# Performance work log

Measured on AMD Instinct MI355X. Metric: run time of the kernel, lower is better.

## Reference

```python
import jax, jax.numpy as jnp
import numpy as np

BLOCK_SIZE = 2048
FRAMES = 4096
BASE_RESONANCE = 0.5
MAX_GAIN = 5.0


def fft_convolve(a, b):
    # Linear convolution via zero-padded FFT, truncated to original length
    # (matches the matching-pursuit repo's fft_convolve).
    n = a.shape[-1]
    fa = jnp.fft.rfft(a, n=2 * n, axis=-1)
    fb = jnp.fft.rfft(b, n=2 * n, axis=-1)
    out = jnp.fft.irfft(fa * fb, n=2 * n, axis=-1)
    return out[..., :n]


def setup_inputs() -> dict:
    key = jax.random.key(0)
    ks = jax.random.split(key, 6)
    cp = jax.random.normal(ks[0], (1, BLOCK_SIZE, FRAMES), dtype=jnp.float32)
    w1 = jax.random.uniform(ks[1], (BLOCK_SIZE, BLOCK_SIZE), jnp.float32, -0.01, 0.01)
    w2 = jax.random.uniform(ks[2], (BLOCK_SIZE, BLOCK_SIZE), jnp.float32, -0.01, 0.01)
    audio = jax.random.uniform(ks[3], (BLOCK_SIZE, BLOCK_SIZE), jnp.float32, -0.01, 0.01)
    decays = jax.random.uniform(ks[4], (BLOCK_SIZE,), jnp.float32, 0.001, 0.99)
    gains = jax.random.uniform(ks[5], (BLOCK_SIZE,), jnp.float32, -3.0, 3.0)
    return {"cp": cp, "w1": w1, "w2": w2, "audio": audio, "decays": decays, "gains": gains}


def reference(cp, w1, w2, audio, decays, gains):
    b, c, frames = cp.shape  # b == 1, c == BLOCK_SIZE
    x0 = jnp.maximum(cp, 0.0)  # torch.relu(cp)
    # decay values in (base_resonance, 1): base + sigmoid(decays) * span
    d = BASE_RESONANCE + jax.nn.sigmoid(decays) * (1.0 - BASE_RESONANCE)  # (c,)
    g = jax.nn.sigmoid(gains) * MAX_GAIN  # (c,)

    x = jnp.einsum('ij,bjt->bit', w1, x0)  # mapping @ control_plane
    orig = x

    # decay envelope: log -> cumsum -> exp over frames => d ** (t+1)
    logd = jnp.log(1e-12 + jnp.broadcast_to(d[None, :, None], (b, c, frames)))
    denv = jnp.exp(jnp.cumsum(logd, axis=-1))  # (b, c, frames)

    x = fft_convolve(x, denv)
    x = jnp.einsum('ij,bjt->bit', w2, x) + orig
    cp_out = jnp.tanh(x * g[None, :, None])

    audio_out = jnp.einsum('wj,bjt->bwt', audio, cp_out)  # (b, window, frames)
    audio_out = jnp.transpose(audio_out, (0, 2, 1)).reshape(b, 1, -1)
    return audio_out, cp_out
```

## Files before the change

kernel.cpp:

```cpp
#include <hip/hip_runtime.h>
#include <math.h>

typedef __attribute__((ext_vector_type(8))) short bf16x8;
typedef __attribute__((ext_vector_type(8))) unsigned short u16x8;
typedef __attribute__((ext_vector_type(4))) unsigned short u16x4;
typedef __attribute__((ext_vector_type(4))) float f32x4;
typedef unsigned short u16;

__device__ __forceinline__ u16 f2bf(float f) {
  unsigned u = __builtin_bit_cast(unsigned, f);
  return (u16)((u + 0x7FFFu + ((u >> 16) & 1u)) >> 16);
}

__device__ __forceinline__ void gload16(const u16* g, u16* l) {
  __builtin_amdgcn_global_load_lds((const __attribute__((address_space(1))) void*)g,
                                   (__attribute__((address_space(3))) void*)l, 16, 0, 0);
}

__device__ __forceinline__ void sbar() {
  __builtin_amdgcn_sched_barrier(0);
  __builtin_amdgcn_s_barrier();
  __builtin_amdgcn_sched_barrier(0);
}

#define VMWAIT(n) asm volatile("s_waitcnt vmcnt(" #n ")" ::: "memory")
#define MFMA16(a, b, c) __builtin_amdgcn_mfma_f32_16x16x32_bf16((a), (b), (c), 0, 0, 0)

__device__ __forceinline__ float decay_of(float d) {
  return 1e-12f + 0.5f + 0.5f / (1.0f + expf(-d));
}

__global__ __launch_bounds__(256) void cvt3_kernel(const float* __restrict__ a,
                                                   const float* __restrict__ b,
                                                   const float* __restrict__ c,
                                                   u16* __restrict__ out) {
  const int i = blockIdx.x * 256 + threadIdx.x;
  const float* src;
  int j = i;
  if (i < 1048576) { src = a; }
  else if (i < 2097152) { src = b; j = i - 1048576; }
  else { src = c; j = i - 2097152; }
  const float4 v = ((const float4*)src)[j];
  u16x4 o = { f2bf(v.x), f2bf(v.y), f2bf(v.z), f2bf(v.w) };
  ((u16x4*)out)[i] = o;
}

__global__ __launch_bounds__(256) void relu_t_kernel(const float* __restrict__ cp,
                                                     u16* __restrict__ x0t) {
  const int cb = blockIdx.x & 31;
  const int tb = blockIdx.x >> 5;
  __shared__ __attribute__((aligned(16))) float tile[64][65];
  const int tid = threadIdx.x;
  const int r0 = tid >> 4, i4 = (tid & 15) * 4;
  #pragma unroll
  for (int rr = 0; rr < 64; rr += 16) {
    const float4 v = *(const float4*)(cp + (size_t)(cb * 64 + r0 + rr) * 4096 + tb * 64 + i4);
    tile[r0 + rr][i4 + 0] = fmaxf(v.x, 0.f);
    tile[r0 + rr][i4 + 1] = fmaxf(v.y, 0.f);
    tile[r0 + rr][i4 + 2] = fmaxf(v.z, 0.f);
    tile[r0 + rr][i4 + 3] = fmaxf(v.w, 0.f);
  }
  __syncthreads();
  #pragma unroll
  for (int it = 0; it < 2; ++it) {
    const int chunk = it * 256 + tid;
    const int i = chunk >> 3, rp = (chunk & 7) * 8;
    u16x8 o;
    #pragma unroll
    for (int q = 0; q < 8; ++q) o[q] = f2bf(tile[rp + q][i]);
    *(u16x8*)(x0t + (size_t)(tb * 64 + i) * 2048 + cb * 64 + rp) = o;
  }
}

__global__ __launch_bounds__(128) void iir_partial_kernel(const float* __restrict__ x,
                                                          const float* __restrict__ decays,
                                                          float* __restrict__ L) {
  const int tid = threadIdx.x;
  const int cb = blockIdx.x & 15;
  const int ck = blockIdx.x >> 4;
  const int c0 = cb * 128, t0 = ck * 64;
  __shared__ __attribute__((aligned(16))) float xs[128][65];
  const float dd = decay_of(decays[c0 + tid]);
  #pragma unroll
  for (int it = 0; it < 16; ++it) {
    const int idx = it * 128 + tid;
    const int r = idx >> 4, iv = (idx & 15) * 4;
    const float4 v = *(const float4*)(x + (size_t)(c0 + r) * 4096 + t0 + iv);
    xs[r][iv + 0] = v.x; xs[r][iv + 1] = v.y; xs[r][iv + 2] = v.z; xs[r][iv + 3] = v.w;
  }
  __syncthreads();
  float yv = 0.0f;
  #pragma unroll
  for (int i = 0; i < 64; ++i) yv = dd * (xs[tid][i] + yv);
  L[ck * 2048 + c0 + tid] = yv;
}

__global__ __launch_bounds__(128) void iir_carry_kernel(const float* __restrict__ L,
                                                        const float* __restrict__ decays,
                                                        float* __restrict__ Cin) {
  const int c = blockIdx.x * 128 + threadIdx.x;
  const float dd = decay_of(decays[c]);
  float A = dd;
  #pragma unroll
  for (int p = 0; p < 6; ++p) A = A * A;
  float carry = 0.0f;
  for (int j = 0; j < 64; ++j) {
    Cin[j * 2048 + c] = carry;
    carry = L[j * 2048 + c] + A * carry;
  }
}

__global__ __launch_bounds__(128) void iir_apply_kernel(const float* __restrict__ x,
                                                        const float* __restrict__ decays,
                                                        const float* __restrict__ Cin,
                                                        u16* __restrict__ yT) {
  const int tid = threadIdx.x;
  const int cb = blockIdx.x & 15;
  const int ck = blockIdx.x >> 4;
  const int c0 = cb * 128, t0 = ck * 64;
  __shared__ __attribute__((aligned(16))) float xs[128][65];
  __shared__ __attribute__((aligned(16))) u16 ys[64][136];
  const float dd = decay_of(decays[c0 + tid]);
  const float carry = Cin[ck * 2048 + c0 + tid];
  #pragma unroll
  for (int it = 0; it < 16; ++it) {
    const int idx = it * 128 + tid;
    const int r = idx >> 4, iv = (idx & 15) * 4;
    const float4 v = *(const float4*)(x + (size_t)(c0 + r) * 4096 + t0 + iv);
    xs[r][iv + 0] = v.x; xs[r][iv + 1] = v.y; xs[r][iv + 2] = v.z; xs[r][iv + 3] = v.w;
  }
  __syncthreads();
  float yv = carry;
  #pragma unroll
  for (int i = 0; i < 64; ++i) {
    yv = dd * (xs[tid][i] + yv);
    ys[i][tid] = f2bf(yv);
  }
  __syncthreads();
  #pragma unroll
  for (int it = 0; it < 8; ++it) {
    const int chunk = it * 128 + tid;
    const int i = chunk >> 4, cpv = (chunk & 15) * 8;
    u16x8 v = *(const u16x8*)&ys[i][cpv];
    *(u16x8*)(yT + (size_t)(t0 + i) * 2048 + c0 + cpv) = v;
  }
}

__device__ __forceinline__ void read_frag(const u16* Ac, const u16* Bc,
                                          int rA0, int rB0, int jk,
                                          bf16x8 (&a)[4], bf16x8 (&b)[4]) {
  #pragma unroll
  for (int i = 0; i < 4; ++i)
    a[i] = *(const bf16x8*)(Ac + (rA0 + i * 16) * 64 + jk * 8);
  #pragma unroll
  for (int i = 0; i < 4; ++i)
    b[i] = *(const bf16x8*)(Bc + (rB0 + i * 16) * 64 + jk * 8);
}

__device__ __forceinline__ void mfma16x(const bf16x8 (&a)[4], const bf16x8 (&b)[4],
                                        f32x4 (&acc)[4][4]) {
  __builtin_amdgcn_s_setprio(1);
  #pragma unroll
  for (int mi = 0; mi < 4; ++mi)
    #pragma unroll
    for (int ni = 0; ni < 4; ++ni)
      acc[mi][ni] = MFMA16(a[mi], b[ni], acc[mi][ni]);
  __builtin_amdgcn_s_setprio(0);
}

template <int MODE>
__global__ __launch_bounds__(256, 2) void gemm_pl_kernel(
    const u16* __restrict__ A, const u16* __restrict__ Bt, float* __restrict__ C,
    int N, int K, int xlogn,
    const float* __restrict__ orig, const float* __restrict__ gains,
    u16* __restrict__ CbT) {
  __shared__ __attribute__((aligned(16))) u16 Asb[2][128 * 64];
  __shared__ __attribute__((aligned(16))) u16 Bsb[2][128 * 64];
  const int tid = threadIdx.x;
  const int l = tid & 63, w = tid >> 6;
  const int xc = blockIdx.x & 7, rblk = blockIdx.x >> 3;
  const int xn = xc & ((1 << xlogn) - 1), xm = xc >> xlogn;
  const int bm = xm * 8 + (rblk >> 3);
  const int bn = xn * 8 + (rblk & 7);
  const int nt = K >> 6;

  const int cs = (l & 7) ^ (l >> 3);
  const int rsub = l >> 3;
  const u16* aS[4]; const u16* bS[4]; int tO[4];
  #pragma unroll
  for (int u = 0; u < 4; ++u) {
    const int rg = (u * 4 + w) * 8 + rsub;
    aS[u] = A  + (size_t)(bm * 128 + rg) * K + cs * 8;
    bS[u] = Bt + (size_t)(bn * 128 + rg) * K + cs * 8;
    tO[u] = (u * 4 + w) * 512;
  }

#define STAGE(bufA, bufB, tt) do {                                        \
    const long so_ = (long)(tt) * 64;                                     \
    gload16(aS[0] + so_, (bufA) + tO[0]); gload16(aS[1] + so_, (bufA) + tO[1]); \
    gload16(aS[2] + so_, (bufA) + tO[2]); gload16(aS[3] + so_, (bufA) + tO[3]); \
    gload16(bS[0] + so_, (bufB) + tO[0]); gload16(bS[1] + so_, (bufB) + tO[1]); \
    gload16(bS[2] + so_, (bufB) + tO[2]); gload16(bS[3] + so_, (bufB) + tO[3]); \
  } while (0)

  STAGE((u16*)Asb[0], (u16*)Bsb[0], 0);
  STAGE((u16*)Asb[1], (u16*)Bsb[1], 1);

  f32x4 acc[4][4];
  #pragma unroll
  for (int i = 0; i < 4; ++i)
    #pragma unroll
    for (int j = 0; j < 4; ++j) acc[i][j] = (f32x4){0.f, 0.f, 0.f, 0.f};

  const int wr = w >> 1, wc = w & 1;
  const int rA0 = wr * 64 + (l & 15);
  const int rB0 = wc * 64 + (l & 15);
  const int jk0 = (l >> 4) ^ (l & 7);
  const int jk1 = ((l >> 4) + 4) ^ (l & 7);

  bf16x8 pa[4], pb[4], qa[4], qb[4];

  VMWAIT(8);
  sbar();
  read_frag((const u16*)Asb[0], (const u16*)Bsb[0], rA0, rB0, jk0, pa, pb);

  for (int h = 0; h < nt; ++h) {
    const u16* Ac = (const u16*)Asb[0] + (h & 1) * 8192;
    const u16* Bc = (const u16*)Bsb[0] + (h & 1) * 8192;
    u16* Anx = (u16*)Asb[0] + (h & 1) * 8192;
    u16* Bnx = (u16*)Bsb[0] + (h & 1) * 8192;
    const u16* An1 = (const u16*)Asb[0] + ((h + 1) & 1) * 8192;
    const u16* Bn1 = (const u16*)Bsb[0] + ((h + 1) & 1) * 8192;

    read_frag(Ac, Bc, rA0, rB0, jk1, qa, qb);
    mfma16x(pa, pb, acc);
    mfma16x(qa, qb, acc);
    VMWAIT(0);
    sbar();
    if (h + 2 < nt) STAGE(Anx, Bnx, h + 2);
    if (h + 1 < nt) read_frag(An1, Bn1, rA0, rB0, jk0, pa, pb);
  }
#undef STAGE

  const int rb = bm * 128 + wr * 64 + ((l >> 4) * 4);
  const int cb = bn * 128 + wc * 64 + (l & 15);
  #pragma unroll
  for (int mi = 0; mi < 4; ++mi) {
    const int row0 = rb + mi * 16;
    float gv[4] = {0.f, 0.f, 0.f, 0.f};
    if (MODE == 1) {
      #pragma unroll
      for (int j = 0; j < 4; ++j) gv[j] = 5.0f / (1.0f + expf(-gains[row0 + j]));
    }
    #pragma unroll
    for (int ni = 0; ni < 4; ++ni) {
      const int col = cb + ni * 16;
      f32x4 v = acc[mi][ni];
      if (MODE == 1) {
        float cpv[4];
        #pragma unroll
        for (int j = 0; j < 4; ++j) {
          float t = v[j] + orig[(size_t)(row0 + j) * N + col];
          cpv[j] = tanhf(t * gv[j]);
          C[(size_t)(row0 + j) * N + col] = cpv[j];
        }
        u16x4 o = { f2bf(cpv[0]), f2bf(cpv[1]), f2bf(cpv[2]), f2bf(cpv[3]) };
        *(u16x4*)(CbT + (size_t)col * 2048 + row0) = o;
      } else {
        #pragma unroll
        for (int j = 0; j < 4; ++j)
          C[(size_t)(row0 + j) * N + col] = v[j];
      }
    }
  }
}

extern "C" void kernel_launch(void* const* d_in, const int* in_sizes, int n_in,
                              void* d_out, int out_size, void* d_ws, size_t ws_size,
                              hipStream_t stream) {
  const float* cp     = (const float*)d_in[0];
  const float* w1     = (const float*)d_in[1];
  const float* w2     = (const float*)d_in[2];
  const float* audio  = (const float*)d_in[3];
  const float* decays = (const float*)d_in[4];
  const float* gains  = (const float*)d_in[5];

  float* out0 = (float*)d_out;
  float* out1 = out0 + (size_t)2048 * 4096;

  char* ws = (char*)d_ws;
  u16*   w1b    = (u16*)(ws);
  u16*   w2b    = (u16*)(ws + 8388608);
  u16*   audiob = (u16*)(ws + 16777216);
  float* orig   = (float*)(ws + 25165824);
  u16*   yT     = (u16*)(ws + 58720256);
  u16*   x0t    = (u16*)(ws + 75497472);
  u16*   cpbT   = x0t;
  float* Lbuf   = (float*)(ws + 75497472);
  float* Cin    = (float*)(ws + 75497472 + 524288);

  cvt3_kernel<<<12288, 256, 0, stream>>>(w1, w2, audio, w1b);
  relu_t_kernel<<<2048, 256, 0, stream>>>(cp, x0t);

  gemm_pl_kernel<0><<<512, 256, 0, stream>>>(w1b, x0t, orig, 4096, 2048, 2,
                                             nullptr, nullptr, nullptr);
  iir_partial_kernel<<<1024, 128, 0, stream>>>(orig, decays, Lbuf);
  iir_carry_kernel<<<16, 128, 0, stream>>>(Lbuf, decays, Cin);
  iir_apply_kernel<<<1024, 128, 0, stream>>>(orig, decays, Cin, yT);
  gemm_pl_kernel<1><<<512, 256, 0, stream>>>(w2b, yT, out1, 4096, 2048, 2,
                                             orig, gains, cpbT);
  gemm_pl_kernel<0><<<512, 256, 0, stream>>>(cpbT, audiob, out0, 2048, 2048, 1,
                                             nullptr, nullptr, nullptr);
}
```

Baseline: 186.5 us.

## Pre-pack B operands into MFMA fragment order and load them straight to registers

The producer kernels (relu transpose, IIR apply, audio convert) now write the GEMM B operands in a fragment-packed layout. Each wave can then load its B fragments with coalesced 16-byte global loads directly into registers, so B no longer passes through LDS. The GEMM main loop is restructured into an even/odd register double buffer for B, while A keeps its LDS double buffer. This halves LDS traffic and footprint, but B fragments are now re-read from global memory/L2 by each wave pair, and the new layout adds more registers and tighter waitcnt bookkeeping.

```diff
diff --git a/kernel.cpp b/kernel.cpp
--- a/kernel.cpp
+++ b/kernel.cpp
@@ -30,23 +30,37 @@
   return 1e-12f + 0.5f + 0.5f / (1.0f + expf(-d));
 }
 
-__global__ __launch_bounds__(256) void cvt3_kernel(const float* __restrict__ a,
+__device__ __forceinline__ size_t pack_idx(int nrow, int k) {
+  const int bn = nrow >> 7, n16 = (nrow >> 4) & 7, row = nrow & 15;
+  const int kt = k >> 6, kh = (k >> 5) & 1, kc = (k >> 3) & 3;
+  return ((((size_t)(bn * 32 + kt) * 8 + n16) * 2 + kh) * 4 + kc) * 16 + row;
+}
+
+__global__ __launch_bounds__(256) void cvt2_kernel(const float* __restrict__ a,
                                                    const float* __restrict__ b,
-                                                   const float* __restrict__ c,
                                                    u16* __restrict__ out) {
   const int i = blockIdx.x * 256 + threadIdx.x;
-  const float* src;
-  int j = i;
-  if (i < 1048576) { src = a; }
-  else if (i < 2097152) { src = b; j = i - 1048576; }
-  else { src = c; j = i - 2097152; }
+  const float* src = (i < 1048576) ? a : b;
+  const int j = (i < 1048576) ? i : i - 1048576;
   const float4 v = ((const float4*)src)[j];
   u16x4 o = { f2bf(v.x), f2bf(v.y), f2bf(v.z), f2bf(v.w) };
   ((u16x4*)out)[i] = o;
 }
 
+__global__ __launch_bounds__(256) void audio_pack_kernel(const float* __restrict__ audio,
+                                                         u16* __restrict__ pack) {
+  const int gid = blockIdx.x * 256 + threadIdx.x;
+  const int j = (gid & 255) * 8;
+  const int wv = gid >> 8;
+  const float4 v0 = *(const float4*)(audio + (size_t)wv * 2048 + j);
+  const float4 v1 = *(const float4*)(audio + (size_t)wv * 2048 + j + 4);
+  u16x8 o = { f2bf(v0.x), f2bf(v0.y), f2bf(v0.z), f2bf(v0.w),
+              f2bf(v1.x), f2bf(v1.y), f2bf(v1.z), f2bf(v1.w) };
+  *(u16x8*)(pack + pack_idx(wv, j) * 8) = o;
+}
+
 __global__ __launch_bounds__(256) void relu_t_kernel(const float* __restrict__ cp,
-                                                     u16* __restrict__ x0t) {
+                                                     u16* __restrict__ x0p) {
   const int cb = blockIdx.x & 31;
   const int tb = blockIdx.x >> 5;
   __shared__ __attribute__((aligned(16))) float tile[64][65];
@@ -68,7 +82,7 @@
     u16x8 o;
     #pragma unroll
     for (int q = 0; q < 8; ++q) o[q] = f2bf(tile[rp + q][i]);
-    *(u16x8*)(x0t + (size_t)(tb * 64 + i) * 2048 + cb * 64 + rp) = o;
+    *(u16x8*)(x0p + pack_idx(tb * 64 + i, cb * 64 + rp) * 8) = o;
   }
 }
 
@@ -113,7 +127,7 @@
 __global__ __launch_bounds__(128) void iir_apply_kernel(const float* __restrict__ x,
                                                         const float* __restrict__ decays,
                                                         const float* __restrict__ Cin,
-                                                        u16* __restrict__ yT) {
+                                                        u16* __restrict__ yp) {
   const int tid = threadIdx.x;
   const int cb = blockIdx.x & 15;
   const int ck = blockIdx.x >> 4;
@@ -142,40 +156,17 @@
     const int chunk = it * 128 + tid;
     const int i = chunk >> 4, cpv = (chunk & 15) * 8;
     u16x8 v = *(const u16x8*)&ys[i][cpv];
-    *(u16x8*)(yT + (size_t)(t0 + i) * 2048 + c0 + cpv) = v;
-  }
-}
-
-__device__ __forceinline__ void read_frag(const u16* Ac, const u16* Bc,
-                                          int rA0, int rB0, int jk,
-                                          bf16x8 (&a)[4], bf16x8 (&b)[4]) {
-  #pragma unroll
-  for (int i = 0; i < 4; ++i)
-    a[i] = *(const bf16x8*)(Ac + (rA0 + i * 16) * 64 + jk * 8);
-  #pragma unroll
-  for (int i = 0; i < 4; ++i)
-    b[i] = *(const bf16x8*)(Bc + (rB0 + i * 16) * 64 + jk * 8);
-}
-
-__device__ __forceinline__ void mfma16x(const bf16x8 (&a)[4], const bf16x8 (&b)[4],
-                                        f32x4 (&acc)[4][4]) {
-  __builtin_amdgcn_s_setprio(1);
-  #pragma unroll
-  for (int mi = 0; mi < 4; ++mi)
-    #pragma unroll
-    for (int ni = 0; ni < 4; ++ni)
-      acc[mi][ni] = MFMA16(a[mi], b[ni], acc[mi][ni]);
-  __builtin_amdgcn_s_setprio(0);
+    *(u16x8*)(yp + pack_idx(t0 + i, c0 + cpv) * 8) = v;
+  }
 }
 
 template <int MODE>
-__global__ __launch_bounds__(256, 2) void gemm_pl_kernel(
-    const u16* __restrict__ A, const u16* __restrict__ Bt, float* __restrict__ C,
+__global__ __launch_bounds__(256, 2) void gemm_bg_kernel(
+    const u16* __restrict__ A, const u16* __restrict__ Bp, float* __restrict__ C,
     int N, int K, int xlogn,
     const float* __restrict__ orig, const float* __restrict__ gains,
     u16* __restrict__ CbT) {
   __shared__ __attribute__((aligned(16))) u16 Asb[2][128 * 64];
-  __shared__ __attribute__((aligned(16))) u16 Bsb[2][128 * 64];
   const int tid = threadIdx.x;
   const int l = tid & 63, w = tid >> 6;
   const int xc = blockIdx.x & 7, rblk = blockIdx.x >> 3;
@@ -186,25 +177,55 @@
 
   const int cs = (l & 7) ^ (l >> 3);
   const int rsub = l >> 3;
-  const u16* aS[4]; const u16* bS[4]; int tO[4];
+  const u16* aS[4]; int tO[4];
   #pragma unroll
   for (int u = 0; u < 4; ++u) {
     const int rg = (u * 4 + w) * 8 + rsub;
-    aS[u] = A  + (size_t)(bm * 128 + rg) * K + cs * 8;
-    bS[u] = Bt + (size_t)(bn * 128 + rg) * K + cs * 8;
+    aS[u] = A + (size_t)(bm * 128 + rg) * K + cs * 8;
     tO[u] = (u * 4 + w) * 512;
   }
 
-#define STAGE(bufA, bufB, tt) do {                                        \
-    const long so_ = (long)(tt) * 64;                                     \
-    gload16(aS[0] + so_, (bufA) + tO[0]); gload16(aS[1] + so_, (bufA) + tO[1]); \
-    gload16(aS[2] + so_, (bufA) + tO[2]); gload16(aS[3] + so_, (bufA) + tO[3]); \
-    gload16(bS[0] + so_, (bufB) + tO[0]); gload16(bS[1] + so_, (bufB) + tO[1]); \
-    gload16(bS[2] + so_, (bufB) + tO[2]); gload16(bS[3] + so_, (bufB) + tO[3]); \
+#define STAGEA(buf, tt) do {                                               \
+    const long so_ = (long)(tt) * 64;                                      \
+    gload16(aS[0] + so_, (buf) + tO[0]); gload16(aS[1] + so_, (buf) + tO[1]); \
+    gload16(aS[2] + so_, (buf) + tO[2]); gload16(aS[3] + so_, (buf) + tO[3]); \
   } while (0)
 
-  STAGE((u16*)Asb[0], (u16*)Bsb[0], 0);
-  STAGE((u16*)Asb[1], (u16*)Bsb[1], 1);
+  const int wr = w >> 1, wc = w & 1;
+  const int rA0 = wr * 64 + (l & 15);
+  const int jk0 = (l >> 4) ^ (l & 7);
+  const int jk1 = ((l >> 4) + 4) ^ (l & 7);
+
+  const u16* bBase = Bp + ((size_t)bn * nt * 8 + wc * 4) * 1024 + (size_t)l * 8;
+
+#define LOADB(dst, tt) do {                                                \
+    const u16* bp_ = bBase + (size_t)(tt) * 8192;                          \
+    dst[0][0] = *(const bf16x8*)(bp_ +    0); dst[0][1] = *(const bf16x8*)(bp_ +  512); \
+    dst[1][0] = *(const bf16x8*)(bp_ + 1024); dst[1][1] = *(const bf16x8*)(bp_ + 1536); \
+    dst[2][0] = *(const bf16x8*)(bp_ + 2048); dst[2][1] = *(const bf16x8*)(bp_ + 2560); \
+    dst[3][0] = *(const bf16x8*)(bp_ + 3072); dst[3][1] = *(const bf16x8*)(bp_ + 3584); \
+  } while (0)
+
+#define COMPUTE(Ab, bfr) do {                                              \
+    bf16x8 af[4][2];                                                       \
+    _Pragma("unroll")                                                      \
+    for (int mi = 0; mi < 4; ++mi) {                                       \
+      af[mi][0] = *(const bf16x8*)((Ab) + (rA0 + mi * 16) * 64 + jk0 * 8); \
+      af[mi][1] = *(const bf16x8*)((Ab) + (rA0 + mi * 16) * 64 + jk1 * 8); \
+    }                                                                      \
+    __builtin_amdgcn_s_setprio(1);                                         \
+    _Pragma("unroll")                                                      \
+    for (int mi = 0; mi < 4; ++mi)                                         \
+      _Pragma("unroll")                                                    \
+      for (int ni = 0; ni < 4; ++ni)                                       \
+        acc[mi][ni] = MFMA16(af[mi][0], bfr[ni][0], acc[mi][ni]);          \
+    _Pragma("unroll")                                                      \
+    for (int mi = 0; mi < 4; ++mi)                                         \
+      _Pragma("unroll")                                                    \
+      for (int ni = 0; ni < 4; ++ni)                                       \
+        acc[mi][ni] = MFMA16(af[mi][1], bfr[ni][1], acc[mi][ni]);          \
+    __builtin_amdgcn_s_setprio(0);                                         \
+  } while (0)
 
   f32x4 acc[4][4];
   #pragma unroll
@@ -212,35 +233,31 @@
     #pragma unroll
     for (int j = 0; j < 4; ++j) acc[i][j] = (f32x4){0.f, 0.f, 0.f, 0.f};
 
-  const int wr = w >> 1, wc = w & 1;
-  const int rA0 = wr * 64 + (l & 15);
-  const int rB0 = wc * 64 + (l & 15);
-  const int jk0 = (l >> 4) ^ (l & 7);
-  const int jk1 = ((l >> 4) + 4) ^ (l & 7);
-
-  bf16x8 pa[4], pb[4], qa[4], qb[4];
-
-  VMWAIT(8);
+  bf16x8 bfE[4][2], bfO[4][2];
+
+  STAGEA((u16*)Asb[0], 0);
+  LOADB(bfE, 0);
+  STAGEA((u16*)Asb[1], 1);
+  VMWAIT(12);
   sbar();
-  read_frag((const u16*)Asb[0], (const u16*)Bsb[0], rA0, rB0, jk0, pa, pb);
-
-  for (int h = 0; h < nt; ++h) {
-    const u16* Ac = (const u16*)Asb[0] + (h & 1) * 8192;
-    const u16* Bc = (const u16*)Bsb[0] + (h & 1) * 8192;
-    u16* Anx = (u16*)Asb[0] + (h & 1) * 8192;
-    u16* Bnx = (u16*)Bsb[0] + (h & 1) * 8192;
-    const u16* An1 = (const u16*)Asb[0] + ((h + 1) & 1) * 8192;
-    const u16* Bn1 = (const u16*)Bsb[0] + ((h + 1) & 1) * 8192;
-
-    read_frag(Ac, Bc, rA0, rB0, jk1, qa, qb);
-    mfma16x(pa, pb, acc);
-    mfma16x(qa, qb, acc);
-    VMWAIT(0);
+
+  for (int t = 0; t < nt; t += 2) {
+    if (t + 1 < nt) LOADB(bfO, t + 1);
+    if (t < nt - 2) { VMWAIT(12); } else { VMWAIT(0); }
+    COMPUTE((const u16*)Asb[0], bfE);
+    if (t < nt - 2) { VMWAIT(8); } else { VMWAIT(0); }
     sbar();
-    if (h + 2 < nt) STAGE(Anx, Bnx, h + 2);
-    if (h + 1 < nt) read_frag(An1, Bn1, rA0, rB0, jk0, pa, pb);
-  }
-#undef STAGE
+    if (t + 2 < nt) STAGEA((u16*)Asb[0], t + 2);
+    if (t + 2 < nt) LOADB(bfE, t + 2);
+    if (t + 1 < nt - 2) { VMWAIT(12); } else { VMWAIT(0); }
+    COMPUTE((const u16*)Asb[1], bfO);
+    if (t + 1 < nt - 2) { VMWAIT(8); } else { VMWAIT(0); }
+    sbar();
+    if (t + 3 < nt) STAGEA((u16*)Asb[1], t + 3);
+  }
+#undef STAGEA
+#undef LOADB
+#undef COMPUTE
 
   const int rb = bm * 128 + wr * 64 + ((l >> 4) * 4);
   const int cb = bn * 128 + wc * 64 + (l & 15);
@@ -291,24 +308,25 @@
   char* ws = (char*)d_ws;
   u16*   w1b    = (u16*)(ws);
   u16*   w2b    = (u16*)(ws + 8388608);
-  u16*   audiob = (u16*)(ws + 16777216);
+  u16*   audp   = (u16*)(ws + 16777216);
   float* orig   = (float*)(ws + 25165824);
-  u16*   yT     = (u16*)(ws + 58720256);
-  u16*   x0t    = (u16*)(ws + 75497472);
-  u16*   cpbT   = x0t;
+  u16*   yp     = (u16*)(ws + 58720256);
+  u16*   x0p    = (u16*)(ws + 75497472);
+  u16*   cpbT   = x0p;
   float* Lbuf   = (float*)(ws + 75497472);
   float* Cin    = (float*)(ws + 75497472 + 524288);
 
-  cvt3_kernel<<<12288, 256, 0, stream>>>(w1, w2, audio, w1b);
-  relu_t_kernel<<<2048, 256, 0, stream>>>(cp, x0t);
-
-  gemm_pl_kernel<0><<<512, 256, 0, stream>>>(w1b, x0t, orig, 4096, 2048, 2,
+  cvt2_kernel<<<8192, 256, 0, stream>>>(w1, w2, w1b);
+  audio_pack_kernel<<<2048, 256, 0, stream>>>(audio, audp);
+  relu_t_kernel<<<2048, 256, 0, stream>>>(cp, x0p);
+
+  gemm_bg_kernel<0><<<512, 256, 0, stream>>>(w1b, x0p, orig, 4096, 2048, 2,
                                              nullptr, nullptr, nullptr);
   iir_partial_kernel<<<1024, 128, 0, stream>>>(orig, decays, Lbuf);
   iir_carry_kernel<<<16, 128, 0, stream>>>(Lbuf, decays, Cin);
-  iir_apply_kernel<<<1024, 128, 0, stream>>>(orig, decays, Cin, yT);
-  gemm_pl_kernel<1><<<512, 256, 0, stream>>>(w2b, yT, out1, 4096, 2048, 2,
+  iir_apply_kernel<<<1024, 128, 0, stream>>>(orig, decays, Cin, yp);
+  gemm_bg_kernel<1><<<512, 256, 0, stream>>>(w2b, yp, out1, 4096, 2048, 2,
                                              orig, gains, cpbT);
-  gemm_pl_kernel<0><<<512, 256, 0, stream>>>(cpbT, audiob, out0, 2048, 2048, 1,
+  gemm_bg_kernel<0><<<512, 256, 0, stream>>>(cpbT, audp, out0, 2048, 2048, 1,
                                              nullptr, nullptr, nullptr);
 }
```

New measurement: 197.6 us. 5.9% more time.

## Fuse IIR partial-sum pass into first GEMM epilogue via LDS staging

Applied to the files above, without the earlier changes.

The first GEMM gets a new MODE 2 epilogue. It stages each 128x128 output tile in shared memory and computes the per-channel 64-frame IIR partial sums directly, so the separate iir_partial kernel and its full re-read of `orig` go away. The carry kernel now rewrites the partials into carries in place, in a buffer aliased onto the output, which removes the extra Cin buffer. In exchange the GEMM's LDS footprint grows slightly and its epilogue gains a block barrier and a serial 64-step recurrence.

```diff
diff --git a/kernel.cpp b/kernel.cpp
--- a/kernel.cpp
+++ b/kernel.cpp
@@ -72,32 +72,8 @@
   }
 }
 
-__global__ __launch_bounds__(128) void iir_partial_kernel(const float* __restrict__ x,
-                                                          const float* __restrict__ decays,
-                                                          float* __restrict__ L) {
-  const int tid = threadIdx.x;
-  const int cb = blockIdx.x & 15;
-  const int ck = blockIdx.x >> 4;
-  const int c0 = cb * 128, t0 = ck * 64;
-  __shared__ __attribute__((aligned(16))) float xs[128][65];
-  const float dd = decay_of(decays[c0 + tid]);
-  #pragma unroll
-  for (int it = 0; it < 16; ++it) {
-    const int idx = it * 128 + tid;
-    const int r = idx >> 4, iv = (idx & 15) * 4;
-    const float4 v = *(const float4*)(x + (size_t)(c0 + r) * 4096 + t0 + iv);
-    xs[r][iv + 0] = v.x; xs[r][iv + 1] = v.y; xs[r][iv + 2] = v.z; xs[r][iv + 3] = v.w;
-  }
-  __syncthreads();
-  float yv = 0.0f;
-  #pragma unroll
-  for (int i = 0; i < 64; ++i) yv = dd * (xs[tid][i] + yv);
-  L[ck * 2048 + c0 + tid] = yv;
-}
-
-__global__ __launch_bounds__(128) void iir_carry_kernel(const float* __restrict__ L,
-                                                        const float* __restrict__ decays,
-                                                        float* __restrict__ Cin) {
+__global__ __launch_bounds__(128) void iir_carry_kernel(float* __restrict__ LC,
+                                                        const float* __restrict__ decays) {
   const int c = blockIdx.x * 128 + threadIdx.x;
   const float dd = decay_of(decays[c]);
   float A = dd;
@@ -105,8 +81,9 @@
   for (int p = 0; p < 6; ++p) A = A * A;
   float carry = 0.0f;
   for (int j = 0; j < 64; ++j) {
-    Cin[j * 2048 + c] = carry;
-    carry = L[j * 2048 + c] + A * carry;
+    const float Lj = LC[j * 2048 + c];
+    LC[j * 2048 + c] = carry;
+    carry = Lj + A * carry;
   }
 }
 
@@ -173,9 +150,12 @@
     const u16* __restrict__ A, const u16* __restrict__ Bt, float* __restrict__ C,
     int N, int K, int xlogn,
     const float* __restrict__ orig, const float* __restrict__ gains,
-    u16* __restrict__ CbT) {
-  __shared__ __attribute__((aligned(16))) u16 Asb[2][128 * 64];
-  __shared__ __attribute__((aligned(16))) u16 Bsb[2][128 * 64];
+    u16* __restrict__ CbT,
+    const float* __restrict__ decays, float* __restrict__ Lout) {
+  __shared__ __attribute__((aligned(16))) char smem[66048];
+  u16* AsB = (u16*)smem;
+  u16* BsB = (u16*)(smem + 32768);
+  float* cst = (float*)smem;
   const int tid = threadIdx.x;
   const int l = tid & 63, w = tid >> 6;
   const int xc = blockIdx.x & 7, rblk = blockIdx.x >> 3;
@@ -203,8 +183,8 @@
     gload16(bS[2] + so_, (bufB) + tO[2]); gload16(bS[3] + so_, (bufB) + tO[3]); \
   } while (0)
 
-  STAGE((u16*)Asb[0], (u16*)Bsb[0], 0);
-  STAGE((u16*)Asb[1], (u16*)Bsb[1], 1);
+  STAGE(AsB, BsB, 0);
+  STAGE(AsB + 8192, BsB + 8192, 1);
 
   f32x4 acc[4][4];
   #pragma unroll
@@ -222,15 +202,15 @@
 
   VMWAIT(8);
   sbar();
-  read_frag((const u16*)Asb[0], (const u16*)Bsb[0], rA0, rB0, jk0, pa, pb);
+  read_frag(AsB, BsB, rA0, rB0, jk0, pa, pb);
 
   for (int h = 0; h < nt; ++h) {
-    const u16* Ac = (const u16*)Asb[0] + (h & 1) * 8192;
-    const u16* Bc = (const u16*)Bsb[0] + (h & 1) * 8192;
-    u16* Anx = (u16*)Asb[0] + (h & 1) * 8192;
-    u16* Bnx = (u16*)Bsb[0] + (h & 1) * 8192;
-    const u16* An1 = (const u16*)Asb[0] + ((h + 1) & 1) * 8192;
-    const u16* Bn1 = (const u16*)Bsb[0] + ((h + 1) & 1) * 8192;
+    const u16* Ac = AsB + (h & 1) * 8192;
+    const u16* Bc = BsB + (h & 1) * 8192;
+    u16* Anx = AsB + (h & 1) * 8192;
+    u16* Bnx = BsB + (h & 1) * 8192;
+    const u16* An1 = AsB + ((h + 1) & 1) * 8192;
+    const u16* Bn1 = BsB + ((h + 1) & 1) * 8192;
 
     read_frag(Ac, Bc, rA0, rB0, jk1, qa, qb);
     mfma16x(pa, pb, acc);
@@ -242,8 +222,10 @@
   }
 #undef STAGE
 
-  const int rb = bm * 128 + wr * 64 + ((l >> 4) * 4);
-  const int cb = bn * 128 + wc * 64 + (l & 15);
+  const int lr0 = wr * 64 + ((l >> 4) * 4);
+  const int lc0 = wc * 64 + (l & 15);
+  const int rb = bm * 128 + lr0;
+  const int cb = bn * 128 + lc0;
   #pragma unroll
   for (int mi = 0; mi < 4; ++mi) {
     const int row0 = rb + mi * 16;
@@ -270,8 +252,24 @@
         #pragma unroll
         for (int j = 0; j < 4; ++j)
           C[(size_t)(row0 + j) * N + col] = v[j];
+        if (MODE == 2) {
+          const int lr = lr0 + mi * 16, lc = lc0 + ni * 16;
+          #pragma unroll
+          for (int j = 0; j < 4; ++j)
+            cst[(lr + j) * 129 + lc] = v[j];
+        }
       }
     }
+  }
+  if (MODE == 2) {
+    __syncthreads();
+    const int ch = tid & 127, ck2 = tid >> 7;
+    const float dd = decay_of(decays[bm * 128 + ch]);
+    const float* row = cst + (size_t)ch * 129 + ck2 * 64;
+    float yv = 0.0f;
+    #pragma unroll
+    for (int i = 0; i < 64; ++i) yv = dd * (row[i] + yv);
+    Lout[(bn * 2 + ck2) * 2048 + bm * 128 + ch] = yv;
   }
 }
 
@@ -296,19 +294,17 @@
   u16*   yT     = (u16*)(ws + 58720256);
   u16*   x0t    = (u16*)(ws + 75497472);
   u16*   cpbT   = x0t;
-  float* Lbuf   = (float*)(ws + 75497472);
-  float* Cin    = (float*)(ws + 75497472 + 524288);
+  float* LC     = out0;
 
   cvt3_kernel<<<12288, 256, 0, stream>>>(w1, w2, audio, w1b);
   relu_t_kernel<<<2048, 256, 0, stream>>>(cp, x0t);
 
-  gemm_pl_kernel<0><<<512, 256, 0, stream>>>(w1b, x0t, orig, 4096, 2048, 2,
-                                             nullptr, nullptr, nullptr);
-  iir_partial_kernel<<<1024, 128, 0, stream>>>(orig, decays, Lbuf);
-  iir_carry_kernel<<<16, 128, 0, stream>>>(Lbuf, decays, Cin);
-  iir_apply_kernel<<<1024, 128, 0, stream>>>(orig, decays, Cin, yT);
+  gemm_pl_kernel<2><<<512, 256, 0, stream>>>(w1b, x0t, orig, 4096, 2048, 2,
+                                             nullptr, nullptr, nullptr, decays, LC);
+  iir_carry_kernel<<<16, 128, 0, stream>>>(LC, decays);
+  iir_apply_kernel<<<1024, 128, 0, stream>>>(orig, decays, LC, yT);
   gemm_pl_kernel<1><<<512, 256, 0, stream>>>(w2b, yT, out1, 4096, 2048, 2,
-                                             orig, gains, cpbT);
+                                             orig, gains, cpbT, nullptr, nullptr);
   gemm_pl_kernel<0><<<512, 256, 0, stream>>>(cpbT, audiob, out0, 2048, 2048, 1,
-                                             nullptr, nullptr, nullptr);
-}
+                                             nullptr, nullptr, nullptr, nullptr, nullptr);
+}
```

New measurement: 167.8 us, median of 2. 10.1% less time.
